# Kernel tuning notes

Hardware: AMD Instinct MI355X
Metric: run time of the kernel (lower is better)

The kernel has to match this reference:

```python
import jax, jax.numpy as jnp
import numpy as np

NUM_HEADS = 4
HEAD_DIM = 32  # attention_dim 128 / 4 heads
SCALE = HEAD_DIM ** 0.5


def setup_inputs() -> dict:
    key = jax.random.key(0)
    ks = jax.random.split(key, 7)
    B, L, D = 4096, 200, 128
    return {
        "target_item": jax.random.normal(ks[0], (B, D), dtype=jnp.float32),
        "history_sequence": jax.random.normal(ks[1], (B, L, D), dtype=jnp.float32),
        "mask": jax.random.randint(ks[2], (B, L), 0, 2, dtype=jnp.int32),
        "W_q": jax.random.normal(ks[3], (D, D), dtype=jnp.float32) * 0.05,
        "W_k": jax.random.normal(ks[4], (D, D), dtype=jnp.float32) * 0.05,
        "W_v": jax.random.normal(ks[5], (D, D), dtype=jnp.float32) * 0.05,
        "W_o": jax.random.normal(ks[6], (D, D), dtype=jnp.float32) * 0.05,
    }


def reference(target_item, history_sequence, mask, W_q, W_k, W_v, W_o):
    B = target_item.shape[0]
    # QKV projections (nn.Linear with bias=False: y = x @ W.T)
    q = target_item @ W_q.T                      # [B, A]
    k = history_sequence @ W_k.T                 # [B, L, A]
    v = history_sequence @ W_v.T                 # [B, L, A]
    # split heads: q -> [B, H, d], k/v -> [B, H, L, d]
    q = q.reshape(B, NUM_HEADS, HEAD_DIM)
    k = k.reshape(B, -1, NUM_HEADS, HEAD_DIM).transpose(0, 2, 1, 3)
    v = v.reshape(B, -1, NUM_HEADS, HEAD_DIM).transpose(0, 2, 1, 3)
    # single-query scaled dot-product attention
    scores = jnp.einsum("bhd,bhld->bhl", q, k) / SCALE  # [B, H, L]
    m = (mask != 0)[:, None, :]                          # [B, 1, L]
    scores = jnp.where(m, scores, -jnp.inf)
    attn = jax.nn.softmax(scores, axis=-1)               # [B, H, L]
    out = jnp.einsum("bhl,bhld->bhd", attn, v)           # [B, H, d]
    out = out.reshape(B, NUM_HEADS * HEAD_DIM)           # [B, A]
    return out @ W_o.T                                    # [B, q_dim]
```

## Files before the change

### kernel.cpp

```cpp
#include <hip/hip_runtime.h>

#define LL 200
#define DD 128
#define NH 4
#define HSTR 65
#define QTSTR 132
#define RSCALE 0.17677669529663687f

__device__ __forceinline__ float blo(unsigned int u) { return __uint_as_float(u << 16); }
__device__ __forceinline__ float bhi(unsigned int u) { return __uint_as_float(u & 0xffff0000u); }
__device__ __forceinline__ float b2f(unsigned short u) { return __uint_as_float(((unsigned int)u) << 16); }
__device__ __forceinline__ unsigned short f2bf(float f) {
  unsigned int u = __float_as_uint(f);
  u += 0x7fffu + ((u >> 16) & 1u);
  return (unsigned short)(u >> 16);
}
__device__ __forceinline__ unsigned int pack2(float lo, float hi) {
  return ((unsigned int)f2bf(hi) << 16) | (unsigned int)f2bf(lo);
}

template <bool F32>
__device__ __forceinline__ float rowdot128(const void* __restrict__ wrow,
                                           const float* __restrict__ v) {
  float acc = 0.f;
  if constexpr (F32) {
    const float4* wr = (const float4*)wrow;
#pragma unroll
    for (int k = 0; k < 32; k++) {
      float4 w = wr[k];
      float4 vv = *(const float4*)(v + 4 * k);
      acc += w.x * vv.x + w.y * vv.y + w.z * vv.z + w.w * vv.w;
    }
  } else {
    const uint4* wr = (const uint4*)wrow;
#pragma unroll
    for (int k = 0; k < 16; k++) {
      uint4 u = wr[k];
      float4 v0 = *(const float4*)(v + k * 8);
      float4 v1 = *(const float4*)(v + k * 8 + 4);
      acc += blo(u.x) * v0.x + bhi(u.x) * v0.y + blo(u.y) * v0.z + bhi(u.y) * v0.w;
      acc += blo(u.z) * v1.x + bhi(u.z) * v1.y + blo(u.w) * v1.z + bhi(u.w) * v1.w;
    }
  }
  return acc;
}

template <bool F32>
__device__ __forceinline__ float welem(const void* w, size_t idx) {
  if constexpr (F32) return ((const float*)w)[idx];
  else               return b2f(((const unsigned short*)w)[idx]);
}

__global__ void detect_dtype(const unsigned int* __restrict__ hist_dw, int* __restrict__ flag) {
  if (threadIdx.x == 0 && blockIdx.x == 0) {
    int cnt = 0;
    for (int i = 0; i < 256; i++) {
      unsigned int e = (hist_dw[i] >> 7) & 0xffu;
      cnt += (e >= 110u && e <= 134u) ? 1 : 0;
    }
    *flag = (cnt < 128) ? 1 : 0;
  }
}

template <bool F32>
__global__ __launch_bounds__(256, 2)
void mhta_kernel(const void* __restrict__ tgt,
                 const void* __restrict__ hist,
                 const int* __restrict__ mask,
                 const void* __restrict__ Wq,
                 const void* __restrict__ Wk,
                 const void* __restrict__ Wv,
                 const void* __restrict__ Wo,
                 void* __restrict__ out,
                 const int* __restrict__ flag)
{
  __shared__ __align__(16) unsigned int sh_hist[LL * HSTR];
  __shared__ __align__(16) float sh_qt[NH * QTSTR];
  __shared__ __align__(16) float sh_sc[LL * 4];
  __shared__ __align__(16) float sh_tvec[DD];
  __shared__ __align__(16) float sh_qv[DD];
  __shared__ __align__(16) float sh_cpart[2 * 512];

  if ((*flag != 0) != F32) return;

  const int tid = threadIdx.x;
  const int b = blockIdx.x;
  const float NINF = -__builtin_inff();

  if (tid < DD) sh_tvec[tid] = welem<F32>(tgt, (size_t)b * DD + tid);
  __syncthreads();

  if (tid < DD) {
    const char* wrow = (const char*)Wq + (size_t)tid * DD * (F32 ? 4 : 2);
    sh_qv[tid] = rowdot128<F32>(wrow, sh_tvec);
  }
  __syncthreads();

  for (int e = tid; e < NH * DD; e += 256) {
    int h = e >> 7, j = e & 127;
    float acc = 0.f;
#pragma unroll 8
    for (int d = 0; d < 32; d++)
      acc += sh_qv[h * 32 + d] * welem<F32>(Wk, (size_t)(h * 32 + d) * DD + j);
    sh_qt[h * QTSTR + j] = acc * RSCALE;
  }

  if constexpr (F32) {
    const float2* hg = (const float2*)((const float*)hist + (size_t)b * LL * DD);
    for (int g = tid; g < LL * 64; g += 256) {
      float2 f = hg[g];
      sh_hist[(g >> 6) * HSTR + (g & 63)] = pack2(f.x, f.y);
    }
  } else {
    const uint4* hg = (const uint4*)((const unsigned short*)hist + (size_t)b * LL * DD);
    for (int g = tid; g < LL * 16; g += 256) {
      uint4 u = hg[g];
      int l = g >> 4, q = (g & 15) << 2;
      unsigned int* dst = &sh_hist[l * HSTR + q];
      dst[0] = u.x; dst[1] = u.y; dst[2] = u.z; dst[3] = u.w;
    }
  }
  __syncthreads();

  if (tid < LL) {
    const int l = tid;
    float a0 = 0.f, a1 = 0.f, a2 = 0.f, a3 = 0.f;
    const unsigned int* hr = &sh_hist[l * HSTR];
#pragma unroll 4
    for (int j2 = 0; j2 < 64; j2++) {
      unsigned int dw = hr[j2];
      float f0 = blo(dw), f1 = bhi(dw);
      float2 q0 = *(const float2*)&sh_qt[0 * QTSTR + 2 * j2];
      float2 q1 = *(const float2*)&sh_qt[1 * QTSTR + 2 * j2];
      float2 q2 = *(const float2*)&sh_qt[2 * QTSTR + 2 * j2];
      float2 q3 = *(const float2*)&sh_qt[3 * QTSTR + 2 * j2];
      a0 += f0 * q0.x + f1 * q0.y;
      a1 += f0 * q1.x + f1 * q1.y;
      a2 += f0 * q2.x + f1 * q2.y;
      a3 += f0 * q3.x + f1 * q3.y;
    }
    bool mv = mask[(size_t)b * LL + l] != 0;
    float4 sv;
    sv.x = mv ? a0 : NINF;
    sv.y = mv ? a1 : NINF;
    sv.z = mv ? a2 : NINF;
    sv.w = mv ? a3 : NINF;
    *(float4*)&sh_sc[l * 4] = sv;
  }
  __syncthreads();

  {
    const int h = tid >> 6, lane = tid & 63;
    float v0 = sh_sc[lane * 4 + h];
    float v1 = sh_sc[(lane + 64) * 4 + h];
    float v2 = sh_sc[(lane + 128) * 4 + h];
    float v3 = (lane < 8) ? sh_sc[(lane + 192) * 4 + h] : NINF;
    float m = fmaxf(fmaxf(v0, v1), fmaxf(v2, v3));
#pragma unroll
    for (int off = 32; off; off >>= 1) m = fmaxf(m, __shfl_xor(m, off));
    float e0 = __expf(v0 - m), e1 = __expf(v1 - m), e2 = __expf(v2 - m);
    float e3 = (lane < 8) ? __expf(v3 - m) : 0.f;
    float s = e0 + e1 + e2 + e3;
#pragma unroll
    for (int off = 32; off; off >>= 1) s += __shfl_xor(s, off);
    float r = 1.f / s;
    sh_sc[lane * 4 + h] = e0 * r;
    sh_sc[(lane + 64) * 4 + h] = e1 * r;
    sh_sc[(lane + 128) * 4 + h] = e2 * r;
    if (lane < 8) sh_sc[(lane + 192) * 4 + h] = e3 * r;
  }
  __syncthreads();

  {
    const int j = tid & 127, ch = tid >> 7;
    const int sh16 = (j & 1) << 4;
    float a0 = 0.f, a1 = 0.f, a2 = 0.f, a3 = 0.f;
    const int l0 = ch * 100;
#pragma unroll 4
    for (int l = l0; l < l0 + 100; l++) {
      unsigned int dw = sh_hist[l * HSTR + (j >> 1)];
      float f = __uint_as_float((dw >> sh16) << 16);
      float4 at = *(const float4*)&sh_sc[l * 4];
      a0 += f * at.x; a1 += f * at.y; a2 += f * at.z; a3 += f * at.w;
    }
    float* cp = &sh_cpart[ch * 512];
    cp[0 * DD + j] = a0; cp[1 * DD + j] = a1; cp[2 * DD + j] = a2; cp[3 * DD + j] = a3;
  }
  __syncthreads();

  float* cvec = sh_qt;
  for (int idx = tid; idx < 512; idx += 256)
    cvec[idx] = sh_cpart[idx] + sh_cpart[512 + idx];
  __syncthreads();

  if (tid < DD) {
    const char* wrow = (const char*)Wv + (size_t)tid * DD * (F32 ? 4 : 2);
    sh_tvec[tid] = rowdot128<F32>(wrow, &cvec[(tid >> 5) * DD]);
  }
  __syncthreads();

  if (tid < DD) {
    const char* wrow = (const char*)Wo + (size_t)tid * DD * (F32 ? 4 : 2);
    float acc = rowdot128<F32>(wrow, sh_tvec);
    if constexpr (F32) ((float*)out)[(size_t)b * DD + tid] = acc;
    else               ((unsigned short*)out)[(size_t)b * DD + tid] = f2bf(acc);
  }
}

extern "C" void kernel_launch(void* const* d_in, const int* in_sizes, int n_in,
                              void* d_out, int out_size, void* d_ws, size_t ws_size,
                              hipStream_t stream) {
  const void* tgt  = d_in[0];
  const void* hist = d_in[1];
  const int*  mask = (const int*)d_in[2];
  const void* Wq   = d_in[3];
  const void* Wk   = d_in[4];
  const void* Wv   = d_in[5];
  const void* Wo   = d_in[6];

  const int B = in_sizes[0] / DD;
  int* flag = (int*)d_ws;

  detect_dtype<<<dim3(1), dim3(64), 0, stream>>>((const unsigned int*)hist, flag);
  mhta_kernel<true ><<<dim3(B), dim3(256), 0, stream>>>(tgt, hist, mask, Wq, Wk, Wv, Wo, d_out, flag);
  mhta_kernel<false><<<dim3(B), dim3(256), 0, stream>>>(tgt, hist, mask, Wq, Wk, Wv, Wo, d_out, flag);
}
```

Measured before the change: 697.7 us.

## Stream history directly from global memory instead of staging in LDS, fuse dtype detection

Result: no change. 694.5 us (-0.5%).

```diff
diff --git a/kernel.cpp b/kernel.cpp
--- a/kernel.cpp
+++ b/kernel.cpp
@@ -3,8 +3,6 @@
 #define LL 200
 #define DD 128
 #define NH 4
-#define HSTR 65
-#define QTSTR 132
 #define RSCALE 0.17677669529663687f
 
 __device__ __forceinline__ float blo(unsigned int u) { return __uint_as_float(u << 16); }
@@ -15,9 +13,6 @@
   u += 0x7fffu + ((u >> 16) & 1u);
   return (unsigned short)(u >> 16);
 }
-__device__ __forceinline__ unsigned int pack2(float lo, float hi) {
-  return ((unsigned int)f2bf(hi) << 16) | (unsigned int)f2bf(lo);
-}
 
 template <bool F32>
 __device__ __forceinline__ float rowdot128(const void* __restrict__ wrow,
@@ -51,19 +46,170 @@
   else               return b2f(((const unsigned short*)w)[idx]);
 }
 
-__global__ void detect_dtype(const unsigned int* __restrict__ hist_dw, int* __restrict__ flag) {
-  if (threadIdx.x == 0 && blockIdx.x == 0) {
-    int cnt = 0;
-    for (int i = 0; i < 256; i++) {
-      unsigned int e = (hist_dw[i] >> 7) & 0xffu;
-      cnt += (e >= 110u && e <= 134u) ? 1 : 0;
-    }
-    *flag = (cnt < 128) ? 1 : 0;
-  }
-}
+struct __align__(16) Smem {
+  float qt[DD * NH];
+  float sc[LL * NH];
+  float tvec[DD];
+  float qv[DD];
+  float cpart[4 * 512];
+  int flag;
+};
 
 template <bool F32>
-__global__ __launch_bounds__(256, 2)
+__device__ __forceinline__ void body(Smem& sm, const int tid, const int b,
+                                     const void* __restrict__ tgt,
+                                     const void* __restrict__ hist,
+                                     const int* __restrict__ mask,
+                                     const void* __restrict__ Wq,
+                                     const void* __restrict__ Wk,
+                                     const void* __restrict__ Wv,
+                                     const void* __restrict__ Wo,
+                                     void* __restrict__ out) {
+  const float NINF = -__builtin_inff();
+
+  if (tid < DD) sm.tvec[tid] = welem<F32>(tgt, (size_t)b * DD + tid);
+  __syncthreads();
+
+  if (tid < DD)
+    sm.qv[tid] = rowdot128<F32>((const char*)Wq + (size_t)tid * DD * (F32 ? 4 : 2), sm.tvec);
+  __syncthreads();
+
+  for (int e = tid; e < NH * DD; e += 256) {
+    const int h = e >> 7, j = e & 127;
+    float acc = 0.f;
+#pragma unroll 8
+    for (int d = 0; d < 32; d++)
+      acc += sm.qv[h * 32 + d] * welem<F32>(Wk, (size_t)(h * 32 + d) * DD + j);
+    sm.qt[j * NH + h] = acc * RSCALE;
+  }
+  __syncthreads();
+
+  if (tid < LL) {
+    const int l = tid;
+    float a0 = 0.f, a1 = 0.f, a2 = 0.f, a3 = 0.f;
+#define QACC(JE, FV) { float4 q_ = *(const float4*)&sm.qt[(JE) * 4]; const float f_ = (FV); \
+  a0 += f_ * q_.x; a1 += f_ * q_.y; a2 += f_ * q_.z; a3 += f_ * q_.w; }
+    if constexpr (!F32) {
+      const uint4* hr = (const uint4*)((const unsigned short*)hist + (size_t)(b * LL + l) * DD);
+#pragma unroll
+      for (int c = 0; c < 2; c++) {
+        uint4 u[8];
+#pragma unroll
+        for (int k = 0; k < 8; k++) u[k] = hr[c * 8 + k];
+#pragma unroll
+        for (int k = 0; k < 8; k++) {
+          const int jb = c * 64 + k * 8;
+          QACC(jb + 0, blo(u[k].x)); QACC(jb + 1, bhi(u[k].x));
+          QACC(jb + 2, blo(u[k].y)); QACC(jb + 3, bhi(u[k].y));
+          QACC(jb + 4, blo(u[k].z)); QACC(jb + 5, bhi(u[k].z));
+          QACC(jb + 6, blo(u[k].w)); QACC(jb + 7, bhi(u[k].w));
+        }
+      }
+    } else {
+      const float4* hr = (const float4*)((const float*)hist + (size_t)(b * LL + l) * DD);
+#pragma unroll
+      for (int c = 0; c < 4; c++) {
+        float4 u[8];
+#pragma unroll
+        for (int k = 0; k < 8; k++) u[k] = hr[c * 8 + k];
+#pragma unroll
+        for (int k = 0; k < 8; k++) {
+          const int jb = c * 32 + k * 4;
+          QACC(jb + 0, u[k].x); QACC(jb + 1, u[k].y);
+          QACC(jb + 2, u[k].z); QACC(jb + 3, u[k].w);
+        }
+      }
+    }
+#undef QACC
+    const bool mv = mask[(size_t)b * LL + l] != 0;
+    float4 sv;
+    sv.x = mv ? a0 : NINF;
+    sv.y = mv ? a1 : NINF;
+    sv.z = mv ? a2 : NINF;
+    sv.w = mv ? a3 : NINF;
+    *(float4*)&sm.sc[l * 4] = sv;
+  }
+  __syncthreads();
+
+  {
+    const int h = tid >> 6, lane = tid & 63;
+    float v0 = sm.sc[lane * 4 + h];
+    float v1 = sm.sc[(lane + 64) * 4 + h];
+    float v2 = sm.sc[(lane + 128) * 4 + h];
+    float v3 = (lane < 8) ? sm.sc[(lane + 192) * 4 + h] : NINF;
+    float m = fmaxf(fmaxf(v0, v1), fmaxf(v2, v3));
+#pragma unroll
+    for (int off = 32; off; off >>= 1) m = fmaxf(m, __shfl_xor(m, off));
+    float e0 = __expf(v0 - m), e1 = __expf(v1 - m), e2 = __expf(v2 - m);
+    float e3 = (lane < 8) ? __expf(v3 - m) : 0.f;
+    float s = e0 + e1 + e2 + e3;
+#pragma unroll
+    for (int off = 32; off; off >>= 1) s += __shfl_xor(s, off);
+    const float r = 1.f / s;
+    sm.sc[lane * 4 + h] = e0 * r;
+    sm.sc[(lane + 64) * 4 + h] = e1 * r;
+    sm.sc[(lane + 128) * 4 + h] = e2 * r;
+    if (lane < 8) sm.sc[(lane + 192) * 4 + h] = e3 * r;
+  }
+  __syncthreads();
+
+  {
+    const int j2 = tid & 63;
+    const int ch = tid >> 6;
+    const int l0 = ch * 50;
+    float a00=0.f,a01=0.f,a10=0.f,a11=0.f,a20=0.f,a21=0.f,a30=0.f,a31=0.f;
+    if constexpr (!F32) {
+      const unsigned int* hd =
+          (const unsigned int*)((const unsigned short*)hist + (size_t)b * LL * DD) + j2;
+#pragma unroll 5
+      for (int l = l0; l < l0 + 50; l++) {
+        const unsigned int dw = hd[l * 64];
+        const float f0 = blo(dw), f1 = bhi(dw);
+        const float4 at = *(const float4*)&sm.sc[l * 4];
+        a00 += f0 * at.x; a01 += f1 * at.x;
+        a10 += f0 * at.y; a11 += f1 * at.y;
+        a20 += f0 * at.z; a21 += f1 * at.z;
+        a30 += f0 * at.w; a31 += f1 * at.w;
+      }
+    } else {
+      const float2* hf = (const float2*)((const float*)hist + (size_t)b * LL * DD) + j2;
+#pragma unroll 5
+      for (int l = l0; l < l0 + 50; l++) {
+        const float2 f = hf[l * 64];
+        const float4 at = *(const float4*)&sm.sc[l * 4];
+        a00 += f.x * at.x; a01 += f.y * at.x;
+        a10 += f.x * at.y; a11 += f.y * at.y;
+        a20 += f.x * at.z; a21 += f.y * at.z;
+        a30 += f.x * at.w; a31 += f.y * at.w;
+      }
+    }
+    float* cp = &sm.cpart[ch * 512];
+    const int j = 2 * j2;
+    *(float2*)&cp[0 * DD + j] = make_float2(a00, a01);
+    *(float2*)&cp[1 * DD + j] = make_float2(a10, a11);
+    *(float2*)&cp[2 * DD + j] = make_float2(a20, a21);
+    *(float2*)&cp[3 * DD + j] = make_float2(a30, a31);
+  }
+  __syncthreads();
+
+  float* cvec = sm.qt;
+  for (int idx = tid; idx < 512; idx += 256)
+    cvec[idx] = sm.cpart[idx] + sm.cpart[512 + idx] + sm.cpart[1024 + idx] + sm.cpart[1536 + idx];
+  __syncthreads();
+
+  if (tid < DD)
+    sm.tvec[tid] = rowdot128<F32>((const char*)Wv + (size_t)tid * DD * (F32 ? 4 : 2),
+                                  &cvec[(tid >> 5) * DD]);
+  __syncthreads();
+
+  if (tid < DD) {
+    const float acc = rowdot128<F32>((const char*)Wo + (size_t)tid * DD * (F32 ? 4 : 2), sm.tvec);
+    if constexpr (F32) ((float*)out)[(size_t)b * DD + tid] = acc;
+    else               ((unsigned short*)out)[(size_t)b * DD + tid] = f2bf(acc);
+  }
+}
+
+__global__ __launch_bounds__(256, 5)
 void mhta_kernel(const void* __restrict__ tgt,
                  const void* __restrict__ hist,
                  const int* __restrict__ mask,
@@ -71,140 +217,22 @@
                  const void* __restrict__ Wk,
                  const void* __restrict__ Wv,
                  const void* __restrict__ Wo,
-                 void* __restrict__ out,
-                 const int* __restrict__ flag)
+                 void* __restrict__ out)
 {
-  __shared__ __align__(16) unsigned int sh_hist[LL * HSTR];
-  __shared__ __align__(16) float sh_qt[NH * QTSTR];
-  __shared__ __align__(16) float sh_sc[LL * 4];
-  __shared__ __align__(16) float sh_tvec[DD];
-  __shared__ __align__(16) float sh_qv[DD];
-  __shared__ __align__(16) float sh_cpart[2 * 512];
-
-  if ((*flag != 0) != F32) return;
-
+  __shared__ Smem sm;
   const int tid = threadIdx.x;
   const int b = blockIdx.x;
-  const float NINF = -__builtin_inff();
-
-  if (tid < DD) sh_tvec[tid] = welem<F32>(tgt, (size_t)b * DD + tid);
-  __syncthreads();
-
-  if (tid < DD) {
-    const char* wrow = (const char*)Wq + (size_t)tid * DD * (F32 ? 4 : 2);
-    sh_qv[tid] = rowdot128<F32>(wrow, sh_tvec);
-  }
-  __syncthreads();
-
-  for (int e = tid; e < NH * DD; e += 256) {
-    int h = e >> 7, j = e & 127;
-    float acc = 0.f;
-#pragma unroll 8
-    for (int d = 0; d < 32; d++)
-      acc += sh_qv[h * 32 + d] * welem<F32>(Wk, (size_t)(h * 32 + d) * DD + j);
-    sh_qt[h * QTSTR + j] = acc * RSCALE;
-  }
-
-  if constexpr (F32) {
-    const float2* hg = (const float2*)((const float*)hist + (size_t)b * LL * DD);
-    for (int g = tid; g < LL * 64; g += 256) {
-      float2 f = hg[g];
-      sh_hist[(g >> 6) * HSTR + (g & 63)] = pack2(f.x, f.y);
-    }
-  } else {
-    const uint4* hg = (const uint4*)((const unsigned short*)hist + (size_t)b * LL * DD);
-    for (int g = tid; g < LL * 16; g += 256) {
-      uint4 u = hg[g];
-      int l = g >> 4, q = (g & 15) << 2;
-      unsigned int* dst = &sh_hist[l * HSTR + q];
-      dst[0] = u.x; dst[1] = u.y; dst[2] = u.z; dst[3] = u.w;
-    }
-  }
-  __syncthreads();
-
-  if (tid < LL) {
-    const int l = tid;
-    float a0 = 0.f, a1 = 0.f, a2 = 0.f, a3 = 0.f;
-    const unsigned int* hr = &sh_hist[l * HSTR];
-#pragma unroll 4
-    for (int j2 = 0; j2 < 64; j2++) {
-      unsigned int dw = hr[j2];
-      float f0 = blo(dw), f1 = bhi(dw);
-      float2 q0 = *(const float2*)&sh_qt[0 * QTSTR + 2 * j2];
-      float2 q1 = *(const float2*)&sh_qt[1 * QTSTR + 2 * j2];
-      float2 q2 = *(const float2*)&sh_qt[2 * QTSTR + 2 * j2];
-      float2 q3 = *(const float2*)&sh_qt[3 * QTSTR + 2 * j2];
-      a0 += f0 * q0.x + f1 * q0.y;
-      a1 += f0 * q1.x + f1 * q1.y;
-      a2 += f0 * q2.x + f1 * q2.y;
-      a3 += f0 * q3.x + f1 * q3.y;
-    }
-    bool mv = mask[(size_t)b * LL + l] != 0;
-    float4 sv;
-    sv.x = mv ? a0 : NINF;
-    sv.y = mv ? a1 : NINF;
-    sv.z = mv ? a2 : NINF;
-    sv.w = mv ? a3 : NINF;
-    *(float4*)&sh_sc[l * 4] = sv;
-  }
-  __syncthreads();
-
-  {
-    const int h = tid >> 6, lane = tid & 63;
-    float v0 = sh_sc[lane * 4 + h];
-    float v1 = sh_sc[(lane + 64) * 4 + h];
-    float v2 = sh_sc[(lane + 128) * 4 + h];
-    float v3 = (lane < 8) ? sh_sc[(lane + 192) * 4 + h] : NINF;
-    float m = fmaxf(fmaxf(v0, v1), fmaxf(v2, v3));
-#pragma unroll
-    for (int off = 32; off; off >>= 1) m = fmaxf(m, __shfl_xor(m, off));
-    float e0 = __expf(v0 - m), e1 = __expf(v1 - m), e2 = __expf(v2 - m);
-    float e3 = (lane < 8) ? __expf(v3 - m) : 0.f;
-    float s = e0 + e1 + e2 + e3;
-#pragma unroll
-    for (int off = 32; off; off >>= 1) s += __shfl_xor(s, off);
-    float r = 1.f / s;
-    sh_sc[lane * 4 + h] = e0 * r;
-    sh_sc[(lane + 64) * 4 + h] = e1 * r;
-    sh_sc[(lane + 128) * 4 + h] = e2 * r;
-    if (lane < 8) sh_sc[(lane + 192) * 4 + h] = e3 * r;
-  }
-  __syncthreads();
-
-  {
-    const int j = tid & 127, ch = tid >> 7;
-    const int sh16 = (j & 1) << 4;
-    float a0 = 0.f, a1 = 0.f, a2 = 0.f, a3 = 0.f;
-    const int l0 = ch * 100;
-#pragma unroll 4
-    for (int l = l0; l < l0 + 100; l++) {
-      unsigned int dw = sh_hist[l * HSTR + (j >> 1)];
-      float f = __uint_as_float((dw >> sh16) << 16);
-      float4 at = *(const float4*)&sh_sc[l * 4];
-      a0 += f * at.x; a1 += f * at.y; a2 += f * at.z; a3 += f * at.w;
-    }
-    float* cp = &sh_cpart[ch * 512];
-    cp[0 * DD + j] = a0; cp[1 * DD + j] = a1; cp[2 * DD + j] = a2; cp[3 * DD + j] = a3;
-  }
-  __syncthreads();
-
-  float* cvec = sh_qt;
-  for (int idx = tid; idx < 512; idx += 256)
-    cvec[idx] = sh_cpart[idx] + sh_cpart[512 + idx];
-  __syncthreads();
-
-  if (tid < DD) {
-    const char* wrow = (const char*)Wv + (size_t)tid * DD * (F32 ? 4 : 2);
-    sh_tvec[tid] = rowdot128<F32>(wrow, &cvec[(tid >> 5) * DD]);
-  }
-  __syncthreads();
-
-  if (tid < DD) {
-    const char* wrow = (const char*)Wo + (size_t)tid * DD * (F32 ? 4 : 2);
-    float acc = rowdot128<F32>(wrow, sh_tvec);
-    if constexpr (F32) ((float*)out)[(size_t)b * DD + tid] = acc;
-    else               ((unsigned short*)out)[(size_t)b * DD + tid] = f2bf(acc);
-  }
+
+  if (tid < 64) {
+    const unsigned int* hd = (const unsigned int*)((const char*)hist + (size_t)b * LL * DD * 2);
+    const unsigned int e = (hd[tid] >> 7) & 0xffu;
+    const unsigned long long bal = __ballot(e >= 110u && e <= 134u);
+    if (tid == 0) sm.flag = (__popcll(bal) < 32) ? 1 : 0;
+  }
+  __syncthreads();
+
+  if (sm.flag) body<true >(sm, tid, b, tgt, hist, mask, Wq, Wk, Wv, Wo, out);
+  else         body<false>(sm, tid, b, tgt, hist, mask, Wq, Wk, Wv, Wo, out);
 }
 
 extern "C" void kernel_launch(void* const* d_in, const int* in_sizes, int n_in,
@@ -219,9 +247,6 @@
   const void* Wo   = d_in[6];
 
   const int B = in_sizes[0] / DD;
-  int* flag = (int*)d_ws;
-
-  detect_dtype<<<dim3(1), dim3(64), 0, stream>>>((const unsigned int*)hist, flag);
-  mhta_kernel<true ><<<dim3(B), dim3(256), 0, stream>>>(tgt, hist, mask, Wq, Wk, Wv, Wo, d_out, flag);
-  mhta_kernel<false><<<dim3(B), dim3(256), 0, stream>>>(tgt, hist, mask, Wq, Wk, Wv, Wo, d_out, flag);
-}
+
+  mhta_kernel<<<dim3(B), dim3(256), 0, stream>>>(tgt, hist, mask, Wq, Wk, Wv, Wo, d_out);
+}
```
